# Kernel optimization log

Measured on AMD Instinct MI355X. Metric: run time of the kernel, lower is better.

Reference implementation:

```python
import jax, jax.numpy as jnp
import numpy as np
from jax import lax

SIGMA = 1.5
WZ, WY, WX = 27, 5, 5
C1 = 0.01 ** 2
C2 = 0.03 ** 2

def _gauss1d(n):
    x = np.arange(n, dtype=np.float64)
    g = np.exp(-(x - n // 2) ** 2 / (2.0 * SIGMA ** 2))
    return (g / g.sum()).astype(np.float32)

_wz = jnp.asarray(_gauss1d(WZ))  # [27]
_wy = jnp.asarray(_gauss1d(WY))  # [5]
_wx = jnp.asarray(_gauss1d(WX))  # [5]

DN = ('NCDHW', 'OIDHW', 'NCDHW')

def _blur(v):
    # Separable anisotropic Gaussian == the outer-product 3D window conv
    v = lax.conv_general_dilated(v, _wz.reshape(1, 1, WZ, 1, 1), (1, 1, 1),
                                 [(WZ // 2, WZ // 2), (0, 0), (0, 0)], dimension_numbers=DN)
    v = lax.conv_general_dilated(v, _wy.reshape(1, 1, 1, WY, 1), (1, 1, 1),
                                 [(0, 0), (WY // 2, WY // 2), (0, 0)], dimension_numbers=DN)
    v = lax.conv_general_dilated(v, _wx.reshape(1, 1, 1, 1, WX), (1, 1, 1),
                                 [(0, 0), (0, 0), (WX // 2, WX // 2)], dimension_numbers=DN)
    return v

def setup_inputs() -> dict:
    key = jax.random.key(0)
    k1, k2 = jax.random.split(key)
    shape = (2, 1, 128, 256, 256)
    img1 = jax.random.uniform(k1, shape, dtype=jnp.float32)
    img2 = jax.random.uniform(k2, shape, dtype=jnp.float32)
    return {"img1": img1, "img2": img2}

def reference(img1, img2):
    mu1 = _blur(img1)
    mu2 = _blur(img2)
    mu1_sq = mu1 * mu1
    mu2_sq = mu2 * mu2
    mu1_mu2 = mu1 * mu2
    sigma1_sq = _blur(img1 * img1) - mu1_sq
    sigma2_sq = _blur(img2 * img2) - mu2_sq
    sigma12 = _blur(img1 * img2) - mu1_mu2
    ssim_map = ((2.0 * mu1_mu2 + C1) * (2.0 * sigma12 + C2)) / \
               ((mu1_sq + mu2_sq + C1) * (sigma1_sq + sigma2_sq + C2))
    return 1.0 - jnp.mean(ssim_map)
```

## Files before the change

kernel.cpp:

```cpp
#include <hip/hip_runtime.h>
#include <hip/hip_fp16.h>
#include <cmath>

#define NB 2
#define NZ 128
#define NY 256
#define NX 256
#define NPLANE (NY * NX)
#define NVOL (NZ * NPLANE)
#define NTOT (NB * NVOL)

#define ZR 6
#define C1F 1.0e-4f
#define C2F 9.0e-4f

struct Weights {
    float wz[2 * ZR + 1];
    float wy[5];
    float wx[5];
};

__global__ __launch_bounds__(256) void zblur_kernel(const float* __restrict__ A,
                                                    const float* __restrict__ B,
                                                    __half* __restrict__ fields,
                                                    size_t fieldStride,
                                                    int b, int zc0, int CZ,
                                                    Weights W)
{
    const int x0 = blockIdx.x * 64;
    const int y  = blockIdx.y;

    __shared__ __half As[140][64];
    __shared__ __half Bs[140][64];

    const size_t basein = (size_t)b * NVOL + (size_t)y * NX + x0;

    #pragma unroll
    for (int k = 0; k < 9; ++k) {
        int i = threadIdx.x + k * 256;
        if (i < 2240) {
            int r = i >> 4, c = (i & 15) << 2;
            int z = r - ZR;
            float4 va = make_float4(0.f, 0.f, 0.f, 0.f), vb = va;
            if ((unsigned)z < NZ) {
                va = *reinterpret_cast<const float4*>(A + basein + (size_t)z * NPLANE + c);
                vb = *reinterpret_cast<const float4*>(B + basein + (size_t)z * NPLANE + c);
            }
            *reinterpret_cast<__half2*>(&As[r][c])     = __floats2half2_rn(va.x, va.y);
            *reinterpret_cast<__half2*>(&As[r][c + 2]) = __floats2half2_rn(va.z, va.w);
            *reinterpret_cast<__half2*>(&Bs[r][c])     = __floats2half2_rn(vb.x, vb.y);
            *reinterpret_cast<__half2*>(&Bs[r][c + 2]) = __floats2half2_rn(vb.z, vb.w);
        }
    }
    __syncthreads();

    const int x = threadIdx.x & 63;
    const int w = threadIdx.x >> 6;

    for (int gi = 0; gi < 4; ++gi) {
        const int z0 = (w + gi * 4) * 8;
        float acc[8][5];
        #pragma unroll
        for (int j = 0; j < 8; ++j)
            #pragma unroll
            for (int f = 0; f < 5; ++f) acc[j][f] = 0.f;

        #pragma unroll
        for (int k = 0; k < 20; ++k) {
            int row = z0 + k;
            float a  = __half2float(As[row][x]);
            float bb = __half2float(Bs[row][x]);
            float aa = a * a, b2 = bb * bb, ab = a * bb;
            #pragma unroll
            for (int j = 0; j < 8; ++j) {
                const int t = k - j;
                if (t >= 0 && t <= 2 * ZR) {
                    float wt = W.wz[t];
                    acc[j][0] = fmaf(wt, a,  acc[j][0]);
                    acc[j][1] = fmaf(wt, bb, acc[j][1]);
                    acc[j][2] = fmaf(wt, aa, acc[j][2]);
                    acc[j][3] = fmaf(wt, b2, acc[j][3]);
                    acc[j][4] = fmaf(wt, ab, acc[j][4]);
                }
            }
        }

        #pragma unroll
        for (int j = 0; j < 8; ++j) {
            int zr = z0 + j - zc0;
            if (zr >= 0 && zr < CZ) {
                size_t o = (size_t)zr * NPLANE + (size_t)y * NX + x0 + x;
                #pragma unroll
                for (int f = 0; f < 5; ++f)
                    fields[(size_t)f * fieldStride + o] = __float2half_rn(acc[j][f]);
            }
        }
    }
}

__global__ __launch_bounds__(256) void yx_ssim_kernel(const __half* __restrict__ F,
                                                      size_t fieldStride,
                                                      float* __restrict__ acc_out,
                                                      Weights W)
{
    const int strip = blockIdx.x;
    const int zc    = blockIdx.y;
    const int tid   = threadIdx.x;
    const int lx    = tid & 31;
    const int xs    = lx * 8;
    const int y0    = strip * 16 + (tid >> 5) * 2;

    const __half* base = F + (size_t)zc * NPLANE;

    float res[5][2][8];

    #pragma unroll
    for (int f = 0; f < 5; ++f) {
        const __half* src = base + (size_t)f * fieldStride;

        uint4 h[6];
        #pragma unroll
        for (int d = 0; d < 6; ++d) {
            int yy = y0 - 2 + d;
            uint4 v = make_uint4(0u, 0u, 0u, 0u);
            if ((unsigned)yy < NY)
                v = *reinterpret_cast<const uint4*>(src + (size_t)yy * NX + xs);
            h[d] = v;
        }

        float T0[8], T1[8];
        #pragma unroll
        for (int j = 0; j < 8; ++j) { T0[j] = 0.f; T1[j] = 0.f; }
        #pragma unroll
        for (int d = 0; d < 6; ++d) {
            const __half2* ph = reinterpret_cast<const __half2*>(&h[d]);
            float v[8];
            #pragma unroll
            for (int q = 0; q < 4; ++q) {
                float2 u = __half22float2(ph[q]);
                v[2 * q] = u.x; v[2 * q + 1] = u.y;
            }
            if (d < 5) {
                float wt = W.wy[d];
                #pragma unroll
                for (int j = 0; j < 8; ++j) T0[j] = fmaf(wt, v[j], T0[j]);
            }
            if (d > 0) {
                float wt = W.wy[d - 1];
                #pragma unroll
                for (int j = 0; j < 8; ++j) T1[j] = fmaf(wt, v[j], T1[j]);
            }
        }

        #pragma unroll
        for (int r = 0; r < 2; ++r) {
            float* T = r ? T1 : T0;
            float sm2 = __shfl_up(T[6], 1, 64);
            float sm1 = __shfl_up(T[7], 1, 64);
            float sp8 = __shfl_down(T[0], 1, 64);
            float sp9 = __shfl_down(T[1], 1, 64);
            float e[12];
            e[0]  = (lx == 0)  ? 0.f : sm2;
            e[1]  = (lx == 0)  ? 0.f : sm1;
            #pragma unroll
            for (int j = 0; j < 8; ++j) e[2 + j] = T[j];
            e[10] = (lx == 31) ? 0.f : sp8;
            e[11] = (lx == 31) ? 0.f : sp9;
            #pragma unroll
            for (int j = 0; j < 8; ++j) {
                float s = 0.f;
                #pragma unroll
                for (int i = 0; i < 5; ++i) s = fmaf(W.wx[i], e[j + i], s);
                res[f][r][j] = s;
            }
        }
    }

    float local = 0.f;
    #pragma unroll
    for (int r = 0; r < 2; ++r)
        #pragma unroll
        for (int j = 0; j < 8; ++j) {
            float mu1 = res[0][r][j], mu2 = res[1][r][j];
            float z11 = res[2][r][j], z22 = res[3][r][j], z12 = res[4][r][j];
            float mu1sq = mu1 * mu1, mu2sq = mu2 * mu2, mu12 = mu1 * mu2;
            float num = (2.f * mu12 + C1F) * (2.f * (z12 - mu12) + C2F);
            float den = (mu1sq + mu2sq + C1F) * ((z11 - mu1sq) + (z22 - mu2sq) + C2F);
            local += __fdividef(num, den);
        }

    #pragma unroll
    for (int off = 32; off; off >>= 1)
        local += __shfl_down(local, off, 64);

    __shared__ float wsum[4];
    int lane = tid & 63, wid = tid >> 6;
    if (lane == 0) wsum[wid] = local;
    __syncthreads();
    if (tid == 0)
        atomicAdd(acc_out, wsum[0] + wsum[1] + wsum[2] + wsum[3]);
}

__global__ void zero_kernel(float* p) { *p = 0.f; }

__global__ void finalize_kernel(const float* __restrict__ acc, float* __restrict__ out)
{
    out[0] = 1.0f - acc[0] * (1.0f / (float)NTOT);
}

extern "C" void kernel_launch(void* const* d_in, const int* in_sizes, int n_in,
                              void* d_out, int out_size, void* d_ws, size_t ws_size,
                              hipStream_t stream)
{
    const float* img1 = (const float*)d_in[0];
    const float* img2 = (const float*)d_in[1];
    float* out = (float*)d_out;

    int CZ = 128;
    while (CZ > 32 && 64 + 5ull * CZ * NPLANE * 2ull > ws_size) CZ >>= 1;

    float*  acc    = (float*)d_ws;
    __half* fields = (__half*)((char*)d_ws + 64);
    const size_t fieldStride = (size_t)CZ * NPLANE;

    Weights W;
    {
        double gz[27], sz = 0.0;
        for (int i = 0; i < 27; ++i) { double d = i - 13; gz[i] = exp(-d * d / 4.5); sz += gz[i]; }
        for (int k = -ZR; k <= ZR; ++k) W.wz[k + ZR] = (float)(gz[k + 13] / sz);
        double gy[5], sy = 0.0;
        for (int i = 0; i < 5; ++i) { double d = i - 2; gy[i] = exp(-d * d / 4.5); sy += gy[i]; }
        for (int i = 0; i < 5; ++i) { W.wy[i] = (float)(gy[i] / sy); W.wx[i] = (float)(gy[i] / sy); }
    }

    zero_kernel<<<1, 1, 0, stream>>>(acc);

    for (int b = 0; b < NB; ++b) {
        for (int z0 = 0; z0 < NZ; z0 += CZ) {
            dim3 g1(NX / 64, NY);
            zblur_kernel<<<g1, 256, 0, stream>>>(img1, img2, fields, fieldStride, b, z0, CZ, W);
            dim3 g2(NY / 16, CZ);
            yx_ssim_kernel<<<g2, 256, 0, stream>>>(fields, fieldStride, acc, W);
        }
    }

    finalize_kernel<<<1, 1, 0, stream>>>(acc, out);
}
```

Baseline: 284.6 us.

## Use packed half2 FMA for z-blur and narrow tiles in both kernels

```diff
diff --git a/kernel.cpp b/kernel.cpp
--- a/kernel.cpp
+++ b/kernel.cpp
@@ -20,107 +20,114 @@
     float wx[5];
 };
 
-__global__ __launch_bounds__(256) void zblur_kernel(const float* __restrict__ A,
-                                                    const float* __restrict__ B,
-                                                    __half* __restrict__ fields,
-                                                    size_t fieldStride,
-                                                    int b, int zc0, int CZ,
-                                                    Weights W)
-{
-    const int x0 = blockIdx.x * 64;
+__global__ __launch_bounds__(256, 5) void zblur_kernel(const float* __restrict__ A,
+                                                       const float* __restrict__ B,
+                                                       __half* __restrict__ fields,
+                                                       size_t fieldStride,
+                                                       int b, int zc0, int CZ,
+                                                       Weights W)
+{
+    const int x0 = blockIdx.x * 32;
     const int y  = blockIdx.y;
 
-    __shared__ __half As[140][64];
-    __shared__ __half Bs[140][64];
+    __shared__ __half2 As2[140][16];
+    __shared__ __half2 Bs2[140][16];
 
     const size_t basein = (size_t)b * NVOL + (size_t)y * NX + x0;
 
     #pragma unroll
-    for (int k = 0; k < 9; ++k) {
+    for (int k = 0; k < 5; ++k) {
         int i = threadIdx.x + k * 256;
-        if (i < 2240) {
-            int r = i >> 4, c = (i & 15) << 2;
+        if (i < 1120) {
+            int r = i >> 3, c4 = (i & 7) * 4;
             int z = r - ZR;
             float4 va = make_float4(0.f, 0.f, 0.f, 0.f), vb = va;
             if ((unsigned)z < NZ) {
-                va = *reinterpret_cast<const float4*>(A + basein + (size_t)z * NPLANE + c);
-                vb = *reinterpret_cast<const float4*>(B + basein + (size_t)z * NPLANE + c);
+                va = *reinterpret_cast<const float4*>(A + basein + (size_t)z * NPLANE + c4);
+                vb = *reinterpret_cast<const float4*>(B + basein + (size_t)z * NPLANE + c4);
             }
-            *reinterpret_cast<__half2*>(&As[r][c])     = __floats2half2_rn(va.x, va.y);
-            *reinterpret_cast<__half2*>(&As[r][c + 2]) = __floats2half2_rn(va.z, va.w);
-            *reinterpret_cast<__half2*>(&Bs[r][c])     = __floats2half2_rn(vb.x, vb.y);
-            *reinterpret_cast<__half2*>(&Bs[r][c + 2]) = __floats2half2_rn(vb.z, vb.w);
-        }
-    }
+            As2[r][c4 >> 1]       = __floats2half2_rn(va.x, va.y);
+            As2[r][(c4 >> 1) + 1] = __floats2half2_rn(va.z, va.w);
+            Bs2[r][c4 >> 1]       = __floats2half2_rn(vb.x, vb.y);
+            Bs2[r][(c4 >> 1) + 1] = __floats2half2_rn(vb.z, vb.w);
+        }
+    }
+
+    __half2 wzh[13];
+    #pragma unroll
+    for (int t = 0; t < 13; ++t) wzh[t] = __float2half2_rn(W.wz[t]);
+
     __syncthreads();
 
-    const int x = threadIdx.x & 63;
-    const int w = threadIdx.x >> 6;
-
-    for (int gi = 0; gi < 4; ++gi) {
-        const int z0 = (w + gi * 4) * 8;
-        float acc[8][5];
-        #pragma unroll
-        for (int j = 0; j < 8; ++j)
-            #pragma unroll
-            for (int f = 0; f < 5; ++f) acc[j][f] = 0.f;
-
-        #pragma unroll
-        for (int k = 0; k < 20; ++k) {
-            int row = z0 + k;
-            float a  = __half2float(As[row][x]);
-            float bb = __half2float(Bs[row][x]);
-            float aa = a * a, b2 = bb * bb, ab = a * bb;
-            #pragma unroll
-            for (int j = 0; j < 8; ++j) {
-                const int t = k - j;
-                if (t >= 0 && t <= 2 * ZR) {
-                    float wt = W.wz[t];
-                    acc[j][0] = fmaf(wt, a,  acc[j][0]);
-                    acc[j][1] = fmaf(wt, bb, acc[j][1]);
-                    acc[j][2] = fmaf(wt, aa, acc[j][2]);
-                    acc[j][3] = fmaf(wt, b2, acc[j][3]);
-                    acc[j][4] = fmaf(wt, ab, acc[j][4]);
-                }
+    const int oct  = threadIdx.x & 3;
+    const int slot = threadIdx.x >> 2;
+
+    #pragma unroll
+    for (int gi = 0; gi < 2; ++gi) {
+        if (gi * 64 >= zc0 + CZ || gi * 64 + 64 <= zc0) continue;
+        const int z = gi * 64 + slot;
+
+        const __half2 hz = __float2half2_rn(0.f);
+        __half2 acc[5][4];
+        #pragma unroll
+        for (int f = 0; f < 5; ++f)
+            #pragma unroll
+            for (int q = 0; q < 4; ++q) acc[f][q] = hz;
+
+        #pragma unroll
+        for (int k = 0; k < 13; ++k) {
+            int row = z + k;
+            uint4 ra = *reinterpret_cast<const uint4*>(&As2[row][oct * 4]);
+            uint4 rb = *reinterpret_cast<const uint4*>(&Bs2[row][oct * 4]);
+            const __half2* ah = reinterpret_cast<const __half2*>(&ra);
+            const __half2* bh = reinterpret_cast<const __half2*>(&rb);
+            __half2 w = wzh[k];
+            #pragma unroll
+            for (int q = 0; q < 4; ++q) {
+                __half2 a  = ah[q];
+                __half2 bb = bh[q];
+                acc[0][q] = __hfma2(w, a, acc[0][q]);
+                acc[1][q] = __hfma2(w, bb, acc[1][q]);
+                acc[2][q] = __hfma2(w, __hmul2(a, a),  acc[2][q]);
+                acc[3][q] = __hfma2(w, __hmul2(bb, bb), acc[3][q]);
+                acc[4][q] = __hfma2(w, __hmul2(a, bb), acc[4][q]);
             }
         }
 
-        #pragma unroll
-        for (int j = 0; j < 8; ++j) {
-            int zr = z0 + j - zc0;
-            if (zr >= 0 && zr < CZ) {
-                size_t o = (size_t)zr * NPLANE + (size_t)y * NX + x0 + x;
-                #pragma unroll
-                for (int f = 0; f < 5; ++f)
-                    fields[(size_t)f * fieldStride + o] = __float2half_rn(acc[j][f]);
-            }
-        }
-    }
-}
-
-__global__ __launch_bounds__(256) void yx_ssim_kernel(const __half* __restrict__ F,
-                                                      size_t fieldStride,
-                                                      float* __restrict__ acc_out,
-                                                      Weights W)
+        int zr = z - zc0;
+        if (zr >= 0 && zr < CZ) {
+            size_t o = (size_t)zr * NPLANE + (size_t)y * NX + x0 + oct * 8;
+            #pragma unroll
+            for (int f = 0; f < 5; ++f)
+                *reinterpret_cast<uint4*>(fields + (size_t)f * fieldStride + o) =
+                    *reinterpret_cast<const uint4*>(&acc[f][0]);
+        }
+    }
+}
+
+__global__ __launch_bounds__(256, 5) void yx_ssim_kernel(const __half* __restrict__ F,
+                                                         size_t fieldStride,
+                                                         float* __restrict__ acc_out,
+                                                         Weights W)
 {
     const int strip = blockIdx.x;
     const int zc    = blockIdx.y;
     const int tid   = threadIdx.x;
     const int lx    = tid & 31;
     const int xs    = lx * 8;
-    const int y0    = strip * 16 + (tid >> 5) * 2;
+    const int y0    = strip * 8 + (tid >> 5);
 
     const __half* base = F + (size_t)zc * NPLANE;
 
-    float res[5][2][8];
+    float res[5][8];
 
     #pragma unroll
     for (int f = 0; f < 5; ++f) {
         const __half* src = base + (size_t)f * fieldStride;
 
-        uint4 h[6];
-        #pragma unroll
-        for (int d = 0; d < 6; ++d) {
+        uint4 h[5];
+        #pragma unroll
+        for (int d = 0; d < 5; ++d) {
             int yy = y0 - 2 + d;
             uint4 v = make_uint4(0u, 0u, 0u, 0u);
             if ((unsigned)yy < NY)
@@ -128,66 +135,51 @@
             h[d] = v;
         }
 
-        float T0[8], T1[8];
-        #pragma unroll
-        for (int j = 0; j < 8; ++j) { T0[j] = 0.f; T1[j] = 0.f; }
-        #pragma unroll
-        for (int d = 0; d < 6; ++d) {
+        float T[8];
+        #pragma unroll
+        for (int j = 0; j < 8; ++j) T[j] = 0.f;
+        #pragma unroll
+        for (int d = 0; d < 5; ++d) {
             const __half2* ph = reinterpret_cast<const __half2*>(&h[d]);
-            float v[8];
+            float wt = W.wy[d];
             #pragma unroll
             for (int q = 0; q < 4; ++q) {
                 float2 u = __half22float2(ph[q]);
-                v[2 * q] = u.x; v[2 * q + 1] = u.y;
+                T[2 * q]     = fmaf(wt, u.x, T[2 * q]);
+                T[2 * q + 1] = fmaf(wt, u.y, T[2 * q + 1]);
             }
-            if (d < 5) {
-                float wt = W.wy[d];
-                #pragma unroll
-                for (int j = 0; j < 8; ++j) T0[j] = fmaf(wt, v[j], T0[j]);
-            }
-            if (d > 0) {
-                float wt = W.wy[d - 1];
-                #pragma unroll
-                for (int j = 0; j < 8; ++j) T1[j] = fmaf(wt, v[j], T1[j]);
-            }
-        }
-
-        #pragma unroll
-        for (int r = 0; r < 2; ++r) {
-            float* T = r ? T1 : T0;
-            float sm2 = __shfl_up(T[6], 1, 64);
-            float sm1 = __shfl_up(T[7], 1, 64);
-            float sp8 = __shfl_down(T[0], 1, 64);
-            float sp9 = __shfl_down(T[1], 1, 64);
-            float e[12];
-            e[0]  = (lx == 0)  ? 0.f : sm2;
-            e[1]  = (lx == 0)  ? 0.f : sm1;
-            #pragma unroll
-            for (int j = 0; j < 8; ++j) e[2 + j] = T[j];
-            e[10] = (lx == 31) ? 0.f : sp8;
-            e[11] = (lx == 31) ? 0.f : sp9;
-            #pragma unroll
-            for (int j = 0; j < 8; ++j) {
-                float s = 0.f;
-                #pragma unroll
-                for (int i = 0; i < 5; ++i) s = fmaf(W.wx[i], e[j + i], s);
-                res[f][r][j] = s;
-            }
+        }
+
+        float sm2 = __shfl_up(T[6], 1, 64);
+        float sm1 = __shfl_up(T[7], 1, 64);
+        float sp8 = __shfl_down(T[0], 1, 64);
+        float sp9 = __shfl_down(T[1], 1, 64);
+        float e[12];
+        e[0]  = (lx == 0)  ? 0.f : sm2;
+        e[1]  = (lx == 0)  ? 0.f : sm1;
+        #pragma unroll
+        for (int j = 0; j < 8; ++j) e[2 + j] = T[j];
+        e[10] = (lx == 31) ? 0.f : sp8;
+        e[11] = (lx == 31) ? 0.f : sp9;
+        #pragma unroll
+        for (int j = 0; j < 8; ++j) {
+            float s = 0.f;
+            #pragma unroll
+            for (int i = 0; i < 5; ++i) s = fmaf(W.wx[i], e[j + i], s);
+            res[f][j] = s;
         }
     }
 
     float local = 0.f;
     #pragma unroll
-    for (int r = 0; r < 2; ++r)
-        #pragma unroll
-        for (int j = 0; j < 8; ++j) {
-            float mu1 = res[0][r][j], mu2 = res[1][r][j];
-            float z11 = res[2][r][j], z22 = res[3][r][j], z12 = res[4][r][j];
-            float mu1sq = mu1 * mu1, mu2sq = mu2 * mu2, mu12 = mu1 * mu2;
-            float num = (2.f * mu12 + C1F) * (2.f * (z12 - mu12) + C2F);
-            float den = (mu1sq + mu2sq + C1F) * ((z11 - mu1sq) + (z22 - mu2sq) + C2F);
-            local += __fdividef(num, den);
-        }
+    for (int j = 0; j < 8; ++j) {
+        float mu1 = res[0][j], mu2 = res[1][j];
+        float z11 = res[2][j], z22 = res[3][j], z12 = res[4][j];
+        float mu1sq = mu1 * mu1, mu2sq = mu2 * mu2, mu12 = mu1 * mu2;
+        float num = (2.f * mu12 + C1F) * (2.f * (z12 - mu12) + C2F);
+        float den = (mu1sq + mu2sq + C1F) * ((z11 - mu1sq) + (z22 - mu2sq) + C2F);
+        local += __fdividef(num, den);
+    }
 
     #pragma unroll
     for (int off = 32; off; off >>= 1)
@@ -237,9 +229,9 @@
 
     for (int b = 0; b < NB; ++b) {
         for (int z0 = 0; z0 < NZ; z0 += CZ) {
-            dim3 g1(NX / 64, NY);
+            dim3 g1(NX / 32, NY);
             zblur_kernel<<<g1, 256, 0, stream>>>(img1, img2, fields, fieldStride, b, z0, CZ, W);
-            dim3 g2(NY / 16, CZ);
+            dim3 g2(NY / 8, CZ);
             yx_ssim_kernel<<<g2, 256, 0, stream>>>(fields, fieldStride, acc, W);
         }
     }
```

Result: slower. 824.2 us (+189.6%).
